# Kernel tuning notes

Hardware: AMD Instinct MI355X
Metric: run time of the kernel (lower is better)

## Reference

```python
import jax, jax.numpy as jnp
import numpy as np

GRID_H, GRID_W = 14, 14  # grid_size from init_kwargs (crop_height, crop_width)


def _bilinear_crop(feature_map, boxes, bbox_idx, crop_h, crop_w):
    """crop_and_resize-style ROIAlign.

    feature_map: [N, C, H, W] float
    boxes:       [M, 4] (x1, y1, x2, y2) in feature-map pixel coords
    bbox_idx:    [M] int32 batch index per box
    returns:     [M, C, crop_h, crop_w]
    """
    N, C, H, W = feature_map.shape
    x1, y1, x2, y2 = boxes[:, 0], boxes[:, 1], boxes[:, 2], boxes[:, 3]

    # Sample points evenly spaced INCLUDING the box corners (tf.crop_and_resize grid).
    ti = jnp.arange(crop_h, dtype=boxes.dtype) / (crop_h - 1)  # [gh]
    tj = jnp.arange(crop_w, dtype=boxes.dtype) / (crop_w - 1)  # [gw]
    ys = y1[:, None] + (y2 - y1)[:, None] * ti  # [M, gh]
    xs = x1[:, None] + (x2 - x1)[:, None] * tj  # [M, gw]

    # Out-of-range samples get extrapolation value 0.
    my = (ys >= 0) & (ys <= H - 1)  # [M, gh]
    mx = (xs >= 0) & (xs <= W - 1)  # [M, gw]

    y0f = jnp.floor(ys)
    x0f = jnp.floor(xs)
    ly = ys - y0f  # [M, gh] lerp weights
    lx = xs - x0f  # [M, gw]

    y0 = jnp.clip(y0f, 0, H - 1).astype(jnp.int32)
    y1i = jnp.clip(y0f + 1, 0, H - 1).astype(jnp.int32)
    x0 = jnp.clip(x0f, 0, W - 1).astype(jnp.int32)
    x1i = jnp.clip(x0f + 1, 0, W - 1).astype(jnp.int32)

    b = bbox_idx[:, None, None]            # [M,1,1]
    Y0, Y1 = y0[:, :, None], y1i[:, :, None]   # [M,gh,1]
    X0, X1 = x0[:, None, :], x1i[:, None, :]   # [M,1,gw]

    # Advanced indexing with the channel slice in the middle -> result [M,gh,gw,C]
    g00 = feature_map[b, :, Y0, X0]
    g01 = feature_map[b, :, Y0, X1]
    g10 = feature_map[b, :, Y1, X0]
    g11 = feature_map[b, :, Y1, X1]

    wy = ly[:, :, None, None]  # [M,gh,1,1]
    wx = lx[:, None, :, None]  # [M,1,gw,1]
    out = (g00 * (1 - wy) * (1 - wx) + g01 * (1 - wy) * wx
           + g10 * wy * (1 - wx) + g11 * wy * wx)  # [M,gh,gw,C]

    mask = (my[:, :, None] & mx[:, None, :])[..., None]  # [M,gh,gw,1]
    out = jnp.where(mask, out, jnp.zeros((), out.dtype))
    return jnp.transpose(out, (0, 3, 1, 2))  # [M,C,gh,gw]


def setup_inputs() -> dict:
    key = jax.random.key(0)
    k1, k2, k3, k4, k5, k6, k7 = jax.random.split(key, 7)
    N, C, H, W = 4, 256, 200, 200
    img = 800  # original image height/width; stride = img / H = 4
    M = 2048

    feature_map = jax.random.normal(k1, (N, C, H, W), dtype=jnp.float32)

    n = jax.random.randint(k2, (M,), 0, N).astype(jnp.float32)
    score = jax.random.uniform(k3, (M,), dtype=jnp.float32)
    x1 = jax.random.uniform(k4, (M,), dtype=jnp.float32, maxval=img * 0.6)
    y1 = jax.random.uniform(k5, (M,), dtype=jnp.float32, maxval=img * 0.6)
    bw = jax.random.uniform(k6, (M,), dtype=jnp.float32, minval=16.0, maxval=img * 0.4)
    bh = jax.random.uniform(k7, (M,), dtype=jnp.float32, minval=16.0, maxval=img * 0.4)
    x2 = jnp.minimum(x1 + bw, img - 1.0)
    y2 = jnp.minimum(y1 + bh, img - 1.0)

    rois = jnp.stack([n, score, x1, y1, x2, y2], axis=1)  # [M, 6]
    return {"feature_map": feature_map, "rois": rois, "img_height": img}


def reference(feature_map, rois, img_height):
    H = feature_map.shape[2]
    stride = img_height / H
    bbox_idx = rois[:, 0].astype(jnp.int32)
    boxes = rois[:, 2:] / stride  # image coords -> feature-map coords
    return _bilinear_crop(feature_map, boxes, bbox_idx, GRID_H, GRID_W)
```

## Files before the change

### kernel.cpp

```cpp
#include <hip/hip_runtime.h>

#define GH 14
#define GW 14
#define CCHUNK 64

__global__ __launch_bounds__(256) void roi_align_kernel(
    const float* __restrict__ fmap,
    const float* __restrict__ rois,
    const int*   __restrict__ imgh,
    float*       __restrict__ out,
    int C, int H, int W)
{
    const int t = threadIdx.x;
    if (t >= GH * GW) return;

    const int m  = blockIdx.y;
    const int c0 = blockIdx.x * CCHUNK;

    const int j = t % GW;
    const int i = t / GW;

    const float stride = (float)imgh[0] / (float)H;

    const float* r = rois + (size_t)m * 6;
    const int   b  = (int)r[0];
    const float x1 = r[2] / stride;
    const float y1 = r[3] / stride;
    const float x2 = r[4] / stride;
    const float y2 = r[5] / stride;

    const float ti = (float)i / (float)(GH - 1);
    const float tj = (float)j / (float)(GW - 1);
    const float ys = y1 + (y2 - y1) * ti;
    const float xs = x1 + (x2 - x1) * tj;

    const bool my = (ys >= 0.0f) && (ys <= (float)(H - 1));
    const bool mx = (xs >= 0.0f) && (xs <= (float)(W - 1));

    const float y0f = floorf(ys);
    const float x0f = floorf(xs);
    const float ly  = ys - y0f;
    const float lx  = xs - x0f;

    const int y0  = (int)fminf(fmaxf(y0f,        0.0f), (float)(H - 1));
    const int y1i = (int)fminf(fmaxf(y0f + 1.0f, 0.0f), (float)(H - 1));
    const int x0  = (int)fminf(fmaxf(x0f,        0.0f), (float)(W - 1));
    const int x1i = (int)fminf(fmaxf(x0f + 1.0f, 0.0f), (float)(W - 1));

    const float msk = (my && mx) ? 1.0f : 0.0f;
    const float w00 = msk * (1.0f - ly) * (1.0f - lx);
    const float w01 = msk * (1.0f - ly) * lx;
    const float w10 = msk * ly * (1.0f - lx);
    const float w11 = msk * ly * lx;

    const int o00 = y0  * W + x0;
    const int o01 = y0  * W + x1i;
    const int o10 = y1i * W + x0;
    const int o11 = y1i * W + x1i;

    const int HW = H * W;
    const float* __restrict__ p = fmap + ((size_t)b * C + c0) * (size_t)HW;
    float*       __restrict__ o = out  + ((size_t)m * C + c0) * (size_t)(GH * GW) + t;

    #pragma unroll 4
    for (int c = 0; c < CCHUNK; ++c) {
        const float g00 = p[o00];
        const float g01 = p[o01];
        const float g10 = p[o10];
        const float g11 = p[o11];
        *o = g00 * w00 + g01 * w01 + g10 * w10 + g11 * w11;
        p += HW;
        o += GH * GW;
    }
}

extern "C" void kernel_launch(void* const* d_in, const int* in_sizes, int n_in,
                              void* d_out, int out_size, void* d_ws, size_t ws_size,
                              hipStream_t stream) {
    const float* fmap = (const float*)d_in[0];
    const float* rois = (const float*)d_in[1];
    const int*   imgh = (const int*)d_in[2];

    float* out = (float*)d_out;

    const int C = 256, H = 200, W = 200;
    const int M = in_sizes[1] / 6;

    dim3 grid(C / CCHUNK, M);
    roi_align_kernel<<<grid, 256, 0, stream>>>(fmap, rois, imgh, out, C, H, W);
}
```

Before: 912.2 us.

## Transpose feature map to NHWC and gather channels coalesced via LDS staging

Adds a tiled NCHW-to-NHWC transpose into workspace, then a gather kernel where each lane handles one channel, so the four bilinear taps read contiguous channel runs instead of strided scattered points. Results are staged in shared memory and written out in NCHW order so the output stores stay coalesced. This costs an extra full pass over the 164 MB feature map each call and relies on the workspace being large enough. If it is not, the original kernel runs as a fallback.

```diff
diff --git a/kernel.cpp b/kernel.cpp
--- a/kernel.cpp
+++ b/kernel.cpp
@@ -2,75 +2,142 @@
 
 #define GH 14
 #define GW 14
-#define CCHUNK 64
 
-__global__ __launch_bounds__(256) void roi_align_kernel(
-    const float* __restrict__ fmap,
+__global__ __launch_bounds__(256) void nchw_to_nhwc_kernel(
+    const float* __restrict__ src, float* __restrict__ dst, int C, int HW)
+{
+    __shared__ float tile[32][33];
+    const int b  = blockIdx.z;
+    const int p0 = blockIdx.x * 32;
+    const int c0 = blockIdx.y * 32;
+    const int tx = threadIdx.x;
+    const int ty = threadIdx.y;
+    const float* s = src + (size_t)b * C * HW;
+    float*       d = dst + (size_t)b * C * HW;
+    #pragma unroll
+    for (int k = 0; k < 4; ++k)
+        tile[ty + k * 8][tx] = s[(size_t)(c0 + ty + k * 8) * HW + p0 + tx];
+    __syncthreads();
+    #pragma unroll
+    for (int k = 0; k < 4; ++k)
+        d[(size_t)(p0 + ty + k * 8) * C + c0 + tx] = tile[tx][ty + k * 8];
+}
+
+__global__ __launch_bounds__(256) void roi_gather_nhwc_kernel(
+    const float* __restrict__ fmapT,
     const float* __restrict__ rois,
     const int*   __restrict__ imgh,
     float*       __restrict__ out,
     int C, int H, int W)
 {
+    __shared__ float lds[64 * 197];
+    const int tid  = threadIdx.x;
+    const int lane = tid & 63;
+    const int wv   = tid >> 6;
+    const int m    = blockIdx.y;
+    const int c0   = blockIdx.x * 64;
+
+    const float stride = (float)imgh[0] / (float)H;
+    const float* r = rois + (size_t)m * 6;
+    const int   b   = (int)r[0];
+    const float rx1 = r[2] / stride;
+    const float ry1 = r[3] / stride;
+    const float rx2 = r[4] / stride;
+    const float ry2 = r[5] / stride;
+
+    const float* __restrict__ base = fmapT + (size_t)b * H * W * C + c0 + lane;
+
+    const float fH = (float)(H - 1), fW = (float)(W - 1);
+
+    #pragma unroll 2
+    for (int k = 0; k < 49; ++k) {
+        const int s = wv * 49 + k;
+        const int i = s / GW;
+        const int j = s - i * GW;
+
+        const float ys = ry1 + (ry2 - ry1) * ((float)i / (float)(GH - 1));
+        const float xs = rx1 + (rx2 - rx1) * ((float)j / (float)(GW - 1));
+
+        const bool my = (ys >= 0.0f) && (ys <= fH);
+        const bool mx = (xs >= 0.0f) && (xs <= fW);
+
+        const float y0f = floorf(ys);
+        const float x0f = floorf(xs);
+        const float ly  = ys - y0f;
+        const float lx  = xs - x0f;
+
+        const int y0  = (int)fminf(fmaxf(y0f,        0.0f), fH);
+        const int y1i = (int)fminf(fmaxf(y0f + 1.0f, 0.0f), fH);
+        const int x0  = (int)fminf(fmaxf(x0f,        0.0f), fW);
+        const int x1i = (int)fminf(fmaxf(x0f + 1.0f, 0.0f), fW);
+
+        const float msk = (my && mx) ? 1.0f : 0.0f;
+        const float w00 = msk * (1.0f - ly) * (1.0f - lx);
+        const float w01 = msk * (1.0f - ly) * lx;
+        const float w10 = msk * ly * (1.0f - lx);
+        const float w11 = msk * ly * lx;
+
+        const int o00 = (y0  * W + x0 ) * C;
+        const int o01 = (y0  * W + x1i) * C;
+        const int o10 = (y1i * W + x0 ) * C;
+        const int o11 = (y1i * W + x1i) * C;
+        const float g00 = base[o00];
+        const float g01 = base[o01];
+        const float g10 = base[o10];
+        const float g11 = base[o11];
+
+        lds[lane * 197 + s] = g00 * w00 + g01 * w01 + g10 * w10 + g11 * w11;
+    }
+    __syncthreads();
+
+    for (int k = tid; k < 64 * GH * GW; k += 256) {
+        const int ch = k / (GH * GW);
+        const int s  = k - ch * (GH * GW);
+        out[((size_t)m * C + c0 + ch) * (GH * GW) + s] = lds[ch * 197 + s];
+    }
+}
+
+#define CCHUNK 64
+__global__ __launch_bounds__(256) void roi_align_fallback(
+    const float* __restrict__ fmap, const float* __restrict__ rois,
+    const int* __restrict__ imgh, float* __restrict__ out, int C, int H, int W)
+{
     const int t = threadIdx.x;
     if (t >= GH * GW) return;
-
-    const int m  = blockIdx.y;
+    const int m = blockIdx.y;
     const int c0 = blockIdx.x * CCHUNK;
-
     const int j = t % GW;
     const int i = t / GW;
-
     const float stride = (float)imgh[0] / (float)H;
-
     const float* r = rois + (size_t)m * 6;
-    const int   b  = (int)r[0];
-    const float x1 = r[2] / stride;
-    const float y1 = r[3] / stride;
-    const float x2 = r[4] / stride;
-    const float y2 = r[5] / stride;
-
-    const float ti = (float)i / (float)(GH - 1);
-    const float tj = (float)j / (float)(GW - 1);
-    const float ys = y1 + (y2 - y1) * ti;
-    const float xs = x1 + (x2 - x1) * tj;
-
+    const int b = (int)r[0];
+    const float x1 = r[2] / stride, y1 = r[3] / stride;
+    const float x2 = r[4] / stride, y2 = r[5] / stride;
+    const float ys = y1 + (y2 - y1) * ((float)i / (float)(GH - 1));
+    const float xs = x1 + (x2 - x1) * ((float)j / (float)(GW - 1));
     const bool my = (ys >= 0.0f) && (ys <= (float)(H - 1));
     const bool mx = (xs >= 0.0f) && (xs <= (float)(W - 1));
-
-    const float y0f = floorf(ys);
-    const float x0f = floorf(xs);
-    const float ly  = ys - y0f;
-    const float lx  = xs - x0f;
-
+    const float y0f = floorf(ys), x0f = floorf(xs);
+    const float ly = ys - y0f, lx = xs - x0f;
     const int y0  = (int)fminf(fmaxf(y0f,        0.0f), (float)(H - 1));
     const int y1i = (int)fminf(fmaxf(y0f + 1.0f, 0.0f), (float)(H - 1));
     const int x0  = (int)fminf(fmaxf(x0f,        0.0f), (float)(W - 1));
     const int x1i = (int)fminf(fmaxf(x0f + 1.0f, 0.0f), (float)(W - 1));
-
     const float msk = (my && mx) ? 1.0f : 0.0f;
     const float w00 = msk * (1.0f - ly) * (1.0f - lx);
     const float w01 = msk * (1.0f - ly) * lx;
     const float w10 = msk * ly * (1.0f - lx);
     const float w11 = msk * ly * lx;
-
-    const int o00 = y0  * W + x0;
-    const int o01 = y0  * W + x1i;
-    const int o10 = y1i * W + x0;
-    const int o11 = y1i * W + x1i;
-
+    const int o00 = y0 * W + x0, o01 = y0 * W + x1i;
+    const int o10 = y1i * W + x0, o11 = y1i * W + x1i;
     const int HW = H * W;
     const float* __restrict__ p = fmap + ((size_t)b * C + c0) * (size_t)HW;
-    float*       __restrict__ o = out  + ((size_t)m * C + c0) * (size_t)(GH * GW) + t;
-
+    float* __restrict__ o = out + ((size_t)m * C + c0) * (size_t)(GH * GW) + t;
     #pragma unroll 4
     for (int c = 0; c < CCHUNK; ++c) {
-        const float g00 = p[o00];
-        const float g01 = p[o01];
-        const float g10 = p[o10];
-        const float g11 = p[o11];
+        const float g00 = p[o00], g01 = p[o01], g10 = p[o10], g11 = p[o11];
         *o = g00 * w00 + g01 * w01 + g10 * w10 + g11 * w11;
-        p += HW;
-        o += GH * GW;
+        p += HW; o += GH * GW;
     }
 }
 
@@ -80,12 +147,21 @@
     const float* fmap = (const float*)d_in[0];
     const float* rois = (const float*)d_in[1];
     const int*   imgh = (const int*)d_in[2];
-
     float* out = (float*)d_out;
 
-    const int C = 256, H = 200, W = 200;
-    const int M = in_sizes[1] / 6;
+    const int C = 256, H = 200, W = 200, N = 4;
+    const int M  = in_sizes[1] / 6;
+    const int HW = H * W;
 
-    dim3 grid(C / CCHUNK, M);
-    roi_align_kernel<<<grid, 256, 0, stream>>>(fmap, rois, imgh, out, C, H, W);
+    const size_t need = (size_t)N * C * HW * sizeof(float);
+    if (ws_size >= need) {
+        float* fmapT = (float*)d_ws;
+        dim3 tgrid(HW / 32, C / 32, N);
+        nchw_to_nhwc_kernel<<<tgrid, dim3(32, 8), 0, stream>>>(fmap, fmapT, C, HW);
+        dim3 ggrid(C / 64, M);
+        roi_gather_nhwc_kernel<<<ggrid, 256, 0, stream>>>(fmapT, rois, imgh, out, C, H, W);
+    } else {
+        dim3 grid(C / CCHUNK, M);
+        roi_align_fallback<<<grid, 256, 0, stream>>>(fmap, rois, imgh, out, C, H, W);
+    }
 }
```

Result: faster. 737.9 us (-19.1%).
